# Kernel tuning notes

Measured on AMD Instinct MI355X. Metric: run time of the kernel, lower is better.

Reference implementation:

```python
import jax, jax.numpy as jnp
import numpy as np

B, LC, LQ = 16, 512, 64
H = 256            # args.hidden_dim (BiLSTM output dim)
D = 4 * H          # feedforward / biaffine input dim
DFF = 512          # args.hidden_dim_ffw
C = 3              # num_labels


def setup_inputs() -> dict:
    key = jax.random.key(0)
    ks = jax.random.split(key, 12)
    sc = 0.02
    return {
        "ctx_emb": jax.random.normal(ks[0], (B, LC, H), jnp.float32),
        "ques_emb": jax.random.normal(ks[1], (B, LQ, H), jnp.float32),
        "w_sim": jax.random.normal(ks[2], (3 * H,), jnp.float32) * sc,
        "W1s": jax.random.normal(ks[3], (D, DFF), jnp.float32) * sc,
        "b1s": jnp.zeros((DFF,), jnp.float32),
        "W2s": jax.random.normal(ks[4], (DFF, D), jnp.float32) * sc,
        "b2s": jnp.zeros((D,), jnp.float32),
        "W1e": jax.random.normal(ks[5], (D, DFF), jnp.float32) * sc,
        "b1e": jnp.zeros((DFF,), jnp.float32),
        "W2e": jax.random.normal(ks[6], (DFF, D), jnp.float32) * sc,
        "b2e": jnp.zeros((D,), jnp.float32),
        "Wb": jax.random.normal(ks[7], (D + 1, C, D + 1), jnp.float32) * sc,
    }


def _ffw(x, W1, b1, W2, b2):
    # FeedforwardLayer: w_2(relu(w_1(x))) (dropout is identity at eval)
    return jnp.maximum(x @ W1 + b1, 0.0) @ W2 + b2


def reference(ctx_emb, ques_emb, w_sim, W1s, b1s, W2s, b2s, W1e, b1e, W2e, b2e, Wb):
    w1, w2, w3 = jnp.split(w_sim, 3)
    # Fused BiDAF trilinear similarity: identical math to
    # Linear(cat([ctx_, ques_, ctx_*ques_], -1)) with weight [w1|w2|w3].
    sim = (ctx_emb @ w1)[:, :, None] + (ques_emb @ w2)[:, None, :] \
        + jnp.einsum('bih,bjh->bij', ctx_emb * w3, ques_emb)      # [B,LC,LQ]
    a = jax.nn.softmax(sim, axis=-1)                               # [B,LC,LQ]
    c2q = jnp.einsum('bij,bjh->bih', a, ques_emb)                  # [B,LC,H]
    b = jax.nn.softmax(jnp.max(sim, axis=2), axis=-1)              # [B,LC]
    q2c = jnp.einsum('bi,bih->bh', b, ctx_emb)[:, None, :]         # [B,1,H] broadcast over LC
    x = jnp.concatenate([ctx_emb, c2q, ctx_emb * c2q, ctx_emb * q2c], axis=2)  # [B,LC,4H]
    start = _ffw(x, W1s, b1s, W2s, b2s)                            # [B,LC,D]
    end = _ffw(x, W1e, b1e, W2e, b2e)                              # [B,LC,D]
    ones = jnp.ones(start.shape[:-1] + (1,), start.dtype)
    s1 = jnp.concatenate([start, ones], axis=-1)                   # [B,LC,D+1]
    e1 = jnp.concatenate([end, ones], axis=-1)                     # [B,LC,D+1]
    # Biaffine: score[b,x,y,c] = s1[b,x] . Wb[:,c,:] . e1[b,y]
    return jnp.einsum('bxi,icj,byj->bxyc', s1, Wb, e1)             # [B,LC,LC,C]
```

## Files before the change

### kernel.cpp

```cpp
#include <hip/hip_runtime.h>
#include <hip/hip_bf16.h>
#include <math.h>

typedef __bf16 bf16_t;
typedef bf16_t bf16x4 __attribute__((ext_vector_type(4)));
typedef bf16_t bf16x8 __attribute__((ext_vector_type(8)));
typedef float f32x4 __attribute__((ext_vector_type(4)));

#define Bsz 16
#define LCc 512
#define LQq 64
#define Hd 256
#define Dd 1024
#define DFFd 512
#define DP1 1025
#define KP 1056
#define NP 1152
#define NROW 8192
#define YC 1536

#define OFF_T    0L
#define OFF_QW2  0L
#define OFF_MROW 4096L
#define OFF_Q2C  (OFF_MROW + 32768L)
#define OFF_C2Q  (OFF_Q2C + 16384L)
#define OFF_XB   (OFF_C2Q + 8388608L)
#define OFF_HBUF (OFF_XB + 16777216L)
#define OFF_W1ST (OFF_HBUF + 8388608L)
#define OFF_W2ST (OFF_W1ST + 1048576L)
#define OFF_W1ET (OFF_W2ST + 1048576L)
#define OFF_W2ET (OFF_W1ET + 1048576L)
#define OFF_S1   51904512L
#define OFF_E1   (OFF_S1 + 17301504L)
#define OFF_WBT  (OFF_E1 + 17301504L)

static __device__ __forceinline__ void gload_lds16(const void* g, void* l) {
    __builtin_amdgcn_global_load_lds(
        (const __attribute__((address_space(1))) void*)g,
        (__attribute__((address_space(3))) void*)l, 16, 0, 0);
}

__global__ __launch_bounds__(256) void k_qw2(const float* __restrict__ ques,
                                             const float* __restrict__ wsim,
                                             float* __restrict__ qw2) {
    int row = blockIdx.x * 4 + (threadIdx.x >> 6);
    int lane = threadIdx.x & 63;
    float4 q = *(const float4*)&ques[(long)row * Hd + lane * 4];
    float4 w = *(const float4*)&wsim[Hd + lane * 4];
    float p = q.x * w.x + q.y * w.y + q.z * w.z + q.w * w.w;
#pragma unroll
    for (int o = 32; o >= 1; o >>= 1) p += __shfl_xor(p, o, 64);
    if (lane == 0) qw2[row] = p;
}

__global__ __launch_bounds__(256) void k_wtrans(const float* __restrict__ in,
                                                bf16_t* __restrict__ out,
                                                int K, int N) {
    __shared__ float tile[32][33];
    int k0 = blockIdx.x * 32, n0 = blockIdx.y * 32;
    int r = threadIdx.x >> 5, c = threadIdx.x & 31;
#pragma unroll
    for (int rr = 0; rr < 32; rr += 8)
        tile[r + rr][c] = in[(long)(k0 + r + rr) * N + n0 + c];
    __syncthreads();
#pragma unroll
    for (int rr = 0; rr < 32; rr += 8)
        out[(long)(n0 + r + rr) * K + k0 + c] = (bf16_t)tile[c][r + rr];
}

__global__ __launch_bounds__(256) void k_wb(const float* __restrict__ Wb,
                                            bf16_t* __restrict__ Wbt) {
    int rowz = blockIdx.x;
    int c = rowz / NP, i = rowz % NP;
    int tid = threadIdx.x;
    bf16_t* orow = Wbt + (long)rowz * KP;
#pragma unroll
    for (int p = 0; p < 2; p++) {
        int j4 = tid + p * 256;
        if (j4 < 264) {
            int j = j4 * 4;
            float x = 0.f, y = 0.f, z = 0.f, w = 0.f;
            if (i < DP1) {
                const float* src = Wb + ((long)i * 3 + c) * DP1 + j;
                if (j + 0 < DP1) x = src[0];
                if (j + 1 < DP1) y = src[1];
                if (j + 2 < DP1) z = src[2];
                if (j + 3 < DP1) w = src[3];
            }
            bf16x4 bv = {(bf16_t)x, (bf16_t)y, (bf16_t)z, (bf16_t)w};
            *(bf16x4*)&orow[j] = bv;
        }
    }
}

__global__ __launch_bounds__(256) void k_initse(bf16_t* __restrict__ s1,
                                                bf16_t* __restrict__ e1) {
    int idx = blockIdx.x * 256 + threadIdx.x;
    long r = idx >> 5; int cc = idx & 31;
    bf16_t v = (bf16_t)(cc == 0 ? 1.0f : 0.0f);
    s1[r * KP + 1024 + cc] = v;
    e1[r * KP + 1024 + cc] = v;
}

__global__ __launch_bounds__(256) void k_attn(const float* __restrict__ ctx,
                                              const float* __restrict__ ques,
                                              const float* __restrict__ wsim,
                                              const float* __restrict__ qw2,
                                              float* __restrict__ c2q,
                                              float* __restrict__ mrow) {
    __shared__ bf16x4 qlds[LQq * 64];
    __shared__ float cw3s[4][Hd];
    __shared__ float awave[4][LQq];
    int b = blockIdx.x >> 5;
    int itile = blockIdx.x & 31;
    int tid = threadIdx.x, wid = tid >> 6, lane = tid & 63;
#pragma unroll
    for (int p = 0; p < 16; p++) {
        int s = tid + p * 256;
        int j = s >> 6, h4s = s & 63;
        int h4 = h4s ^ (j & 15);
        float4 v = *(const float4*)&ques[((long)b * LQq + j) * Hd + h4 * 4];
        bf16x4 bv = {(bf16_t)v.x, (bf16_t)v.y, (bf16_t)v.z, (bf16_t)v.w};
        qlds[s] = bv;
    }
    float qw2r = qw2[b * LQq + lane];
    float4 w1v = *(const float4*)&wsim[lane * 4];
    float4 w3v = *(const float4*)&wsim[2 * Hd + lane * 4];
    __syncthreads();
    for (int rr = 0; rr < 4; rr++) {
        int i = itile * 16 + wid * 4 + rr;
        float4 cv = *(const float4*)&ctx[((long)b * LCc + i) * Hd + lane * 4];
        float cw1p = cv.x * w1v.x + cv.y * w1v.y + cv.z * w1v.z + cv.w * w1v.w;
        float4 c3;
        c3.x = cv.x * w3v.x; c3.y = cv.y * w3v.y;
        c3.z = cv.z * w3v.z; c3.w = cv.w * w3v.w;
        *(float4*)&cw3s[wid][lane * 4] = c3;
#pragma unroll
        for (int o = 32; o >= 1; o >>= 1) cw1p += __shfl_xor(cw1p, o, 64);
        __syncthreads();
        float s = cw1p + qw2r;
#pragma unroll 8
        for (int h4 = 0; h4 < 64; h4++) {
            float4 c3v = *(const float4*)&cw3s[wid][h4 * 4];
            bf16x4 qb = qlds[lane * 64 + (h4 ^ (lane & 15))];
            s += c3v.x * (float)qb[0] + c3v.y * (float)qb[1]
               + c3v.z * (float)qb[2] + c3v.w * (float)qb[3];
        }
        float mx = s;
#pragma unroll
        for (int o = 32; o >= 1; o >>= 1) mx = fmaxf(mx, __shfl_xor(mx, o, 64));
        if (lane == 0) mrow[b * LCc + i] = mx;
        float pe = __expf(s - mx);
        float den = pe;
#pragma unroll
        for (int o = 32; o >= 1; o >>= 1) den += __shfl_xor(den, o, 64);
        awave[wid][lane] = pe / den;
        __syncthreads();
        float4 accv = {0.f, 0.f, 0.f, 0.f};
#pragma unroll 8
        for (int j = 0; j < 64; j++) {
            float aj = awave[wid][j];
            bf16x4 qb = qlds[j * 64 + (lane ^ (j & 15))];
            accv.x = fmaf(aj, (float)qb[0], accv.x);
            accv.y = fmaf(aj, (float)qb[1], accv.y);
            accv.z = fmaf(aj, (float)qb[2], accv.z);
            accv.w = fmaf(aj, (float)qb[3], accv.w);
        }
        *(float4*)&c2q[((long)b * LCc + i) * Hd + lane * 4] = accv;
        __syncthreads();
    }
}

__global__ __launch_bounds__(256) void k_q2c(const float* __restrict__ ctx,
                                             const float* __restrict__ mrow,
                                             float* __restrict__ q2c) {
    __shared__ float wbuf[LCc];
    __shared__ float red[8];
    int b = blockIdx.x, tid = threadIdx.x;
    float v0 = mrow[b * LCc + tid], v1 = mrow[b * LCc + 256 + tid];
    float m = fmaxf(v0, v1);
#pragma unroll
    for (int o = 32; o >= 1; o >>= 1) m = fmaxf(m, __shfl_xor(m, o, 64));
    if ((tid & 63) == 0) red[tid >> 6] = m;
    __syncthreads();
    float M = fmaxf(fmaxf(red[0], red[1]), fmaxf(red[2], red[3]));
    float e0 = __expf(v0 - M), e1v = __expf(v1 - M);
    float sm = e0 + e1v;
#pragma unroll
    for (int o = 32; o >= 1; o >>= 1) sm += __shfl_xor(sm, o, 64);
    if ((tid & 63) == 0) red[4 + (tid >> 6)] = sm;
    __syncthreads();
    float S = red[4] + red[5] + red[6] + red[7];
    wbuf[tid] = e0 / S;
    wbuf[tid + 256] = e1v / S;
    __syncthreads();
    float acc = 0.f;
#pragma unroll 8
    for (int i = 0; i < LCc; i++)
        acc = fmaf(wbuf[i], ctx[((long)b * LCc + i) * Hd + tid], acc);
    q2c[b * Hd + tid] = acc;
}

__global__ __launch_bounds__(256) void k_buildx(const float* __restrict__ ctx,
                                                const float* __restrict__ c2q,
                                                const float* __restrict__ q2c,
                                                bf16_t* __restrict__ xb) {
    long r = blockIdx.x;
    int b = (int)(r >> 9);
    int tid = threadIdx.x;
    int sec = tid >> 6, h4 = tid & 63;
    float4 cv = *(const float4*)&ctx[r * Hd + h4 * 4];
    float4 v;
    if (sec == 0) {
        v = cv;
    } else if (sec == 1) {
        v = *(const float4*)&c2q[r * Hd + h4 * 4];
    } else if (sec == 2) {
        float4 q = *(const float4*)&c2q[r * Hd + h4 * 4];
        v.x = cv.x * q.x; v.y = cv.y * q.y; v.z = cv.z * q.z; v.w = cv.w * q.w;
    } else {
        float4 q = *(const float4*)&q2c[b * Hd + h4 * 4];
        v.x = cv.x * q.x; v.y = cv.y * q.y; v.z = cv.z * q.z; v.w = cv.w * q.w;
    }
    bf16x4 bv = {(bf16_t)v.x, (bf16_t)v.y, (bf16_t)v.z, (bf16_t)v.w};
    *(bf16x4*)&xb[r * Dd + sec * Hd + h4 * 4] = bv;
}

template <int MODE>
__global__ __launch_bounds__(256, 2) void gemm_nt(
    const bf16_t* __restrict__ A, const bf16_t* __restrict__ B,
    const float* __restrict__ bias, void* __restrict__ C,
    int K, int lda, int ldb, long sAz, long sBz) {
    __shared__ bf16_t As[128 * 32];
    __shared__ bf16_t Bs[128 * 32];
    int tid = threadIdx.x;
    int wid = tid >> 6, lane = tid & 63;
    const bf16_t* Ab = A + (long)blockIdx.z * sAz + (long)blockIdx.x * 128 * lda;
    const bf16_t* Bb = B + (long)blockIdx.z * sBz + (long)blockIdx.y * 128 * ldb;
    int wr = (wid >> 1) * 64, wc = (wid & 1) * 64;
    int fr = lane & 15, kg = lane >> 4;
    f32x4 acc[4][4] = {};
    for (int k0 = 0; k0 < K; k0 += 32) {
        __syncthreads();
#pragma unroll
        for (int p = 0; p < 2; p++) {
            int q = tid + p * 256;
            int row = q >> 2, cg = q & 3;
            gload_lds16(Ab + (long)row * lda + k0 + cg * 8, &As[q * 8]);
            gload_lds16(Bb + (long)row * ldb + k0 + cg * 8, &Bs[q * 8]);
        }
        __syncthreads();
        bf16x8 af[4], bq[4];
#pragma unroll
        for (int m = 0; m < 4; m++)
            af[m] = *(const bf16x8*)&As[(wr + m * 16 + fr) * 32 + kg * 8];
#pragma unroll
        for (int n = 0; n < 4; n++)
            bq[n] = *(const bf16x8*)&Bs[(wc + n * 16 + fr) * 32 + kg * 8];
#pragma unroll
        for (int m = 0; m < 4; m++)
#pragma unroll
            for (int n = 0; n < 4; n++)
                acc[m][n] = __builtin_amdgcn_mfma_f32_16x16x32_bf16(
                    af[m], bq[n], acc[m][n], 0, 0, 0);
    }
    int g4 = (lane >> 4) * 4;
#pragma unroll
    for (int m = 0; m < 4; m++) {
#pragma unroll
        for (int g = 0; g < 4; g++) {
            long r = (long)blockIdx.x * 128 + wr + m * 16 + g4 + g;
#pragma unroll
            for (int n = 0; n < 4; n++) {
                int col = blockIdx.y * 128 + wc + n * 16 + fr;
                float v = acc[m][n][g];
                if (MODE == 0) {
                    v += bias[col];
                    v = fmaxf(v, 0.f);
                    ((bf16_t*)C)[r * DFFd + col] = (bf16_t)v;
                } else if (MODE == 1) {
                    v += bias[col];
                    ((bf16_t*)C)[r * KP + col] = (bf16_t)v;
                } else if (MODE == 2) {
                    if (col < KP)
                        ((bf16_t*)C)[(r * 3 + blockIdx.z) * KP + col] = (bf16_t)v;
                } else {
                    ((float*)C)[(long)blockIdx.z * (LCc * YC) + r * YC + col] = v;
                }
            }
        }
    }
}

extern "C" void kernel_launch(void* const* d_in, const int* in_sizes, int n_in,
                              void* d_out, int out_size, void* d_ws, size_t ws_size,
                              hipStream_t stream) {
    const float* ctx  = (const float*)d_in[0];
    const float* ques = (const float*)d_in[1];
    const float* wsim = (const float*)d_in[2];
    const float* W1s  = (const float*)d_in[3];
    const float* b1s  = (const float*)d_in[4];
    const float* W2s  = (const float*)d_in[5];
    const float* b2s  = (const float*)d_in[6];
    const float* W1e  = (const float*)d_in[7];
    const float* b1e  = (const float*)d_in[8];
    const float* W2e  = (const float*)d_in[9];
    const float* b2e  = (const float*)d_in[10];
    const float* Wb   = (const float*)d_in[11];

    char* ws = (char*)d_ws;
    float*  qw2  = (float*)(ws + OFF_QW2);
    float*  mrow = (float*)(ws + OFF_MROW);
    float*  q2c  = (float*)(ws + OFF_Q2C);
    float*  c2q  = (float*)(ws + OFF_C2Q);
    bf16_t* xb   = (bf16_t*)(ws + OFF_XB);
    bf16_t* hbuf = (bf16_t*)(ws + OFF_HBUF);
    bf16_t* W1st = (bf16_t*)(ws + OFF_W1ST);
    bf16_t* W2st = (bf16_t*)(ws + OFF_W2ST);
    bf16_t* W1et = (bf16_t*)(ws + OFF_W1ET);
    bf16_t* W2et = (bf16_t*)(ws + OFF_W2ET);
    bf16_t* T    = (bf16_t*)(ws + OFF_T);
    bf16_t* s1   = (bf16_t*)(ws + OFF_S1);
    bf16_t* e1   = (bf16_t*)(ws + OFF_E1);
    bf16_t* Wbt  = (bf16_t*)(ws + OFF_WBT);

    k_qw2<<<256, 256, 0, stream>>>(ques, wsim, qw2);
    k_wtrans<<<dim3(32, 16), 256, 0, stream>>>(W1s, W1st, 1024, 512);
    k_wtrans<<<dim3(16, 32), 256, 0, stream>>>(W2s, W2st, 512, 1024);
    k_wtrans<<<dim3(32, 16), 256, 0, stream>>>(W1e, W1et, 1024, 512);
    k_wtrans<<<dim3(16, 32), 256, 0, stream>>>(W2e, W2et, 512, 1024);
    k_wb<<<3 * NP, 256, 0, stream>>>(Wb, Wbt);
    k_attn<<<Bsz * 32, 256, 0, stream>>>(ctx, ques, wsim, qw2, c2q, mrow);
    k_q2c<<<Bsz, 256, 0, stream>>>(ctx, mrow, q2c);
    k_buildx<<<NROW, 256, 0, stream>>>(ctx, c2q, q2c, xb);
    k_initse<<<1024, 256, 0, stream>>>(s1, e1);

    gemm_nt<0><<<dim3(64, 4, 1), 256, 0, stream>>>(xb, W1st, b1s, hbuf, 1024, 1024, 1024, 0, 0);
    gemm_nt<1><<<dim3(64, 8, 1), 256, 0, stream>>>(hbuf, W2st, b2s, s1, 512, 512, 512, 0, 0);
    gemm_nt<0><<<dim3(64, 4, 1), 256, 0, stream>>>(xb, W1et, b1e, hbuf, 1024, 1024, 1024, 0, 0);
    gemm_nt<1><<<dim3(64, 8, 1), 256, 0, stream>>>(hbuf, W2et, b2e, e1, 512, 512, 512, 0, 0);
    gemm_nt<2><<<dim3(64, 9, 3), 256, 0, stream>>>(e1, Wbt, nullptr, T, KP, KP, KP,
                                                   0, (long)NP * KP);
    gemm_nt<3><<<dim3(4, 12, Bsz), 256, 0, stream>>>(s1, T, nullptr, d_out, KP, KP, KP,
                                                     (long)LCc * KP, (long)YC * KP);
}
```

Measured before the change: 359.4 us.

## Replace biaffine GEMMs with 256x256 double-buffered swizzled 8-wave kernel

Adds a new 512-thread GEMM kernel with 256x256 tiles, 64-wide K steps, XOR-swizzled LDS, double-buffered global-to-LDS loads interleaved with MFMA phases, and an XCD-aware workgroup remap. It is used for the two biaffine GEMMs (e1·Wb and s1·T). The K padding grows from 1056 to 1152 and N padding from 1152 to 1280 so the tiles divide evenly, which adds padded work and larger s1/e1 buffers. The aim is more data reuse per tile and overlap of memory loads with matrix math.

```diff
diff --git a/kernel.cpp b/kernel.cpp
--- a/kernel.cpp
+++ b/kernel.cpp
@@ -14,8 +14,10 @@
 #define Dd 1024
 #define DFFd 512
 #define DP1 1025
-#define KP 1056
-#define NP 1152
+#define KP 1152
+#define NT 18
+#define NIT 9
+#define NP 1280
 #define NROW 8192
 #define YC 1536
 
@@ -30,9 +32,9 @@
 #define OFF_W2ST (OFF_W1ST + 1048576L)
 #define OFF_W1ET (OFF_W2ST + 1048576L)
 #define OFF_W2ET (OFF_W1ET + 1048576L)
-#define OFF_S1   51904512L
-#define OFF_E1   (OFF_S1 + 17301504L)
-#define OFF_WBT  (OFF_E1 + 17301504L)
+#define OFF_S1   56623104L
+#define OFF_E1   (OFF_S1 + 18874368L)
+#define OFF_WBT  (OFF_E1 + 18874368L)
 
 static __device__ __forceinline__ void gload_lds16(const void* g, void* l) {
     __builtin_amdgcn_global_load_lds(
@@ -77,7 +79,7 @@
 #pragma unroll
     for (int p = 0; p < 2; p++) {
         int j4 = tid + p * 256;
-        if (j4 < 264) {
+        if (j4 < KP / 4) {
             int j = j4 * 4;
             float x = 0.f, y = 0.f, z = 0.f, w = 0.f;
             if (i < DP1) {
@@ -96,7 +98,7 @@
 __global__ __launch_bounds__(256) void k_initse(bf16_t* __restrict__ s1,
                                                 bf16_t* __restrict__ e1) {
     int idx = blockIdx.x * 256 + threadIdx.x;
-    long r = idx >> 5; int cc = idx & 31;
+    long r = idx >> 7; int cc = idx & 127;
     bf16_t v = (bf16_t)(cc == 0 ? 1.0f : 0.0f);
     s1[r * KP + 1024 + cc] = v;
     e1[r * KP + 1024 + cc] = v;
@@ -230,13 +232,13 @@
 __global__ __launch_bounds__(256, 2) void gemm_nt(
     const bf16_t* __restrict__ A, const bf16_t* __restrict__ B,
     const float* __restrict__ bias, void* __restrict__ C,
-    int K, int lda, int ldb, long sAz, long sBz) {
+    int K, int lda, int ldb) {
     __shared__ bf16_t As[128 * 32];
     __shared__ bf16_t Bs[128 * 32];
     int tid = threadIdx.x;
     int wid = tid >> 6, lane = tid & 63;
-    const bf16_t* Ab = A + (long)blockIdx.z * sAz + (long)blockIdx.x * 128 * lda;
-    const bf16_t* Bb = B + (long)blockIdx.z * sBz + (long)blockIdx.y * 128 * ldb;
+    const bf16_t* Ab = A + (long)blockIdx.x * 128 * lda;
+    const bf16_t* Bb = B + (long)blockIdx.y * 128 * ldb;
     int wr = (wid >> 1) * 64, wc = (wid & 1) * 64;
     int fr = lane & 15, kg = lane >> 4;
     f32x4 acc[4][4] = {};
@@ -273,19 +275,172 @@
 #pragma unroll
             for (int n = 0; n < 4; n++) {
                 int col = blockIdx.y * 128 + wc + n * 16 + fr;
-                float v = acc[m][n][g];
+                float v = acc[m][n][g] + bias[col];
                 if (MODE == 0) {
-                    v += bias[col];
                     v = fmaxf(v, 0.f);
                     ((bf16_t*)C)[r * DFFd + col] = (bf16_t)v;
-                } else if (MODE == 1) {
-                    v += bias[col];
+                } else {
                     ((bf16_t*)C)[r * KP + col] = (bf16_t)v;
-                } else if (MODE == 2) {
+                }
+            }
+        }
+    }
+}
+
+template <int MODE>
+__global__ __launch_bounds__(512) void gemm8(
+    const bf16_t* __restrict__ A, const bf16_t* __restrict__ B,
+    void* __restrict__ C, int nbx, int nby) {
+    __shared__ char smem[131072];
+    int tid = threadIdx.x;
+    const int nz = (MODE == 2) ? 3 : Bsz;
+    int nwg = nbx * nby * nz;
+    int nper = nwg >> 3;
+    int wg = blockIdx.x;
+    int wgid = (wg & 7) * nper + (wg >> 3);
+    int z = wgid / (nbx * nby);
+    int rem = wgid - z * nbx * nby;
+    int by = rem / nbx, bx = rem - by * nbx;
+    const bf16_t* At;
+    const bf16_t* Bt;
+    if (MODE == 2) {
+        At = A + (long)bx * 256 * KP;
+        Bt = B + ((long)z * NP + by * 256) * KP;
+    } else {
+        At = A + ((long)z * LCc + bx * 256) * KP;
+        Bt = B + ((long)z * YC + by * 256) * KP;
+    }
+    int lane = tid & 63, wv = tid >> 6, wm = wv >> 2, wn = wv & 3;
+    int fr = lane & 15, kg = lane >> 4;
+    int row0 = tid >> 3, sc0 = (tid & 7) ^ (row0 & 7);
+    int q1 = tid + 512;
+    int row1 = q1 >> 3, sc1 = (q1 & 7) ^ (row1 & 7);
+
+    auto STAGE = [&](int mat, int ht, int tile) {
+        int ts = tile <= NT - 1 ? tile : NT - 1;
+        int buf = tile & 1;
+        const bf16_t* base = mat ? Bt : At;
+        long rb = (long)ht * 128;
+        const bf16_t* g0 = base + (rb + row0) * KP + ts * 64 + sc0 * 8;
+        const bf16_t* g1 = base + (rb + row1) * KP + ts * 64 + sc1 * 8;
+        char* l = smem + (mat ? 65536 : 0) + buf * 32768 + ht * 16384;
+        gload_lds16(g0, l + tid * 16);
+        gload_lds16(g1, l + 8192 + tid * 16);
+    };
+    auto RDA = [&](int buf, int h, int m, int kk) -> bf16x8 {
+        int row = wm * 128 + h * 64 + m * 16 + fr;
+        int c16 = kk * 4 + kg;
+        int off = buf * 32768 + row * 128 + ((c16 ^ (row & 7)) << 4);
+        return *(const bf16x8*)(smem + off);
+    };
+    auto RDB = [&](int buf, int v, int n, int kk) -> bf16x8 {
+        int row = wn * 64 + v * 32 + n * 16 + fr;
+        int c16 = kk * 4 + kg;
+        int off = 65536 + buf * 32768 + row * 128 + ((c16 ^ (row & 7)) << 4);
+        return *(const bf16x8*)(smem + off);
+    };
+
+    f32x4 acc[8][4] = {};
+
+    STAGE(0, 0, 0); STAGE(0, 1, 0); STAGE(1, 0, 0); STAGE(1, 1, 0);
+    STAGE(0, 0, 1); STAGE(0, 1, 1);
+    asm volatile("s_waitcnt vmcnt(4)" ::: "memory");
+    __builtin_amdgcn_s_barrier();
+
+    auto doTile = [&](int buf, int sB, int sA, bool boundary) {
+        bf16x8 aL[4][2], aH[4][2], bE[2][2], bO[2][2];
+#pragma unroll
+        for (int m = 0; m < 4; m++)
+#pragma unroll
+            for (int k = 0; k < 2; k++) aL[m][k] = RDA(buf, 0, m, k);
+#pragma unroll
+        for (int n = 0; n < 2; n++)
+#pragma unroll
+            for (int k = 0; k < 2; k++) bE[n][k] = RDB(buf, 0, n, k);
+        STAGE(1, 0, sB);
+        __builtin_amdgcn_s_barrier();
+        __builtin_amdgcn_s_setprio(1);
+#pragma unroll
+        for (int m = 0; m < 4; m++)
+#pragma unroll
+            for (int n = 0; n < 2; n++)
+#pragma unroll
+                for (int k = 0; k < 2; k++)
+                    acc[m][n] = __builtin_amdgcn_mfma_f32_16x16x32_bf16(
+                        aL[m][k], bE[n][k], acc[m][n], 0, 0, 0);
+        __builtin_amdgcn_s_setprio(0);
+        __builtin_amdgcn_s_barrier();
+#pragma unroll
+        for (int n = 0; n < 2; n++)
+#pragma unroll
+            for (int k = 0; k < 2; k++) bO[n][k] = RDB(buf, 1, n, k);
+        STAGE(1, 1, sB);
+        __builtin_amdgcn_s_barrier();
+        __builtin_amdgcn_s_setprio(1);
+#pragma unroll
+        for (int m = 0; m < 4; m++)
+#pragma unroll
+            for (int n = 0; n < 2; n++)
+#pragma unroll
+                for (int k = 0; k < 2; k++)
+                    acc[m][2 + n] = __builtin_amdgcn_mfma_f32_16x16x32_bf16(
+                        aL[m][k], bO[n][k], acc[m][2 + n], 0, 0, 0);
+        __builtin_amdgcn_s_setprio(0);
+        __builtin_amdgcn_s_barrier();
+#pragma unroll
+        for (int m = 0; m < 4; m++)
+#pragma unroll
+            for (int k = 0; k < 2; k++) aH[m][k] = RDA(buf, 1, m, k);
+        STAGE(0, 0, sA);
+        __builtin_amdgcn_s_barrier();
+        __builtin_amdgcn_s_setprio(1);
+#pragma unroll
+        for (int m = 0; m < 4; m++)
+#pragma unroll
+            for (int n = 0; n < 2; n++)
+#pragma unroll
+                for (int k = 0; k < 2; k++)
+                    acc[4 + m][n] = __builtin_amdgcn_mfma_f32_16x16x32_bf16(
+                        aH[m][k], bE[n][k], acc[4 + m][n], 0, 0, 0);
+        __builtin_amdgcn_s_setprio(0);
+        __builtin_amdgcn_s_barrier();
+        STAGE(0, 1, sA);
+        __builtin_amdgcn_s_barrier();
+        __builtin_amdgcn_s_setprio(1);
+#pragma unroll
+        for (int m = 0; m < 4; m++)
+#pragma unroll
+            for (int n = 0; n < 2; n++)
+#pragma unroll
+                for (int k = 0; k < 2; k++)
+                    acc[4 + m][2 + n] = __builtin_amdgcn_mfma_f32_16x16x32_bf16(
+                        aH[m][k], bO[n][k], acc[4 + m][2 + n], 0, 0, 0);
+        __builtin_amdgcn_s_setprio(0);
+        asm volatile("s_waitcnt vmcnt(4)" ::: "memory");
+        __builtin_amdgcn_s_barrier();
+        (void)boundary;
+    };
+
+    for (int it = 0; it < NIT; ++it) {
+        int t = 2 * it;
+        doTile(0, t + 1, t + 2, false);
+        doTile(1, t + 2, t + 3, true);
+    }
+
+#pragma unroll
+    for (int mf = 0; mf < 8; mf++) {
+#pragma unroll
+        for (int g = 0; g < 4; g++) {
+            long r = (long)bx * 256 + wm * 128 + mf * 16 + kg * 4 + g;
+#pragma unroll
+            for (int nf = 0; nf < 4; nf++) {
+                int col = by * 256 + wn * 64 + nf * 16 + fr;
+                float v = acc[mf][nf][g];
+                if (MODE == 2) {
                     if (col < KP)
-                        ((bf16_t*)C)[(r * 3 + blockIdx.z) * KP + col] = (bf16_t)v;
+                        ((bf16_t*)C)[(r * 3 + z) * (long)KP + col] = (bf16_t)v;
                 } else {
-                    ((float*)C)[(long)blockIdx.z * (LCc * YC) + r * YC + col] = v;
+                    ((float*)C)[(long)z * (LCc * YC) + r * YC + col] = v;
                 }
             }
         }
@@ -333,14 +488,12 @@
     k_attn<<<Bsz * 32, 256, 0, stream>>>(ctx, ques, wsim, qw2, c2q, mrow);
     k_q2c<<<Bsz, 256, 0, stream>>>(ctx, mrow, q2c);
     k_buildx<<<NROW, 256, 0, stream>>>(ctx, c2q, q2c, xb);
-    k_initse<<<1024, 256, 0, stream>>>(s1, e1);
-
-    gemm_nt<0><<<dim3(64, 4, 1), 256, 0, stream>>>(xb, W1st, b1s, hbuf, 1024, 1024, 1024, 0, 0);
-    gemm_nt<1><<<dim3(64, 8, 1), 256, 0, stream>>>(hbuf, W2st, b2s, s1, 512, 512, 512, 0, 0);
-    gemm_nt<0><<<dim3(64, 4, 1), 256, 0, stream>>>(xb, W1et, b1e, hbuf, 1024, 1024, 1024, 0, 0);
-    gemm_nt<1><<<dim3(64, 8, 1), 256, 0, stream>>>(hbuf, W2et, b2e, e1, 512, 512, 512, 0, 0);
-    gemm_nt<2><<<dim3(64, 9, 3), 256, 0, stream>>>(e1, Wbt, nullptr, T, KP, KP, KP,
-                                                   0, (long)NP * KP);
-    gemm_nt<3><<<dim3(4, 12, Bsz), 256, 0, stream>>>(s1, T, nullptr, d_out, KP, KP, KP,
-                                                     (long)LCc * KP, (long)YC * KP);
-}
+    k_initse<<<4096, 256, 0, stream>>>(s1, e1);
+
+    gemm_nt<0><<<dim3(64, 4), 256, 0, stream>>>(xb, W1st, b1s, hbuf, 1024, 1024, 1024);
+    gemm_nt<1><<<dim3(64, 8), 256, 0, stream>>>(hbuf, W2st, b2s, s1, 512, 512, 512);
+    gemm_nt<0><<<dim3(64, 4), 256, 0, stream>>>(xb, W1et, b1e, hbuf, 1024, 1024, 1024);
+    gemm_nt<1><<<dim3(64, 8), 256, 0, stream>>>(hbuf, W2et, b2e, e1, 512, 512, 512);
+    gemm8<2><<<480, 512, 0, stream>>>(e1, Wbt, T, 32, 5);
+    gemm8<3><<<192, 512, 0, stream>>>(s1, T, d_out, 2, 6);
+}
```

New measurement: 358.6 us. About the same (-0.2%).
